# Performance work log

Hardware: AMD Instinct MI355X
Metric: run time of the kernel (lower is better)

The kernel has to match this reference:

```python
import jax, jax.numpy as jnp
import numpy as np


def setup_inputs() -> dict:
    key = jax.random.key(0)
    k1, k2 = jax.random.split(key)
    B, N, M, D = 4, 8192, 8192, 3
    ground_truth = jax.random.normal(k1, (B, N, D), dtype=jnp.float32)
    reconstruction = jax.random.normal(k2, (B, M, D), dtype=jnp.float32)
    return {"ground_truth": ground_truth, "reconstruction": reconstruction}


def reference(ground_truth, reconstruction):
    x, y = ground_truth, reconstruction  # [B,N,D], [B,M,D]
    xx = jnp.sum(x * x, axis=-1)                      # [B,N]
    yy = jnp.sum(y * y, axis=-1)                      # [B,M]
    xy = jnp.einsum('bnd,bmd->bnm', x, y)             # [B,N,M]
    P = xx[:, :, None] + yy[:, None, :] - 2.0 * xy    # [B,N,M]
    # clamp(min=1e-10) then mean, in both directions
    loss_1 = jnp.mean(jnp.maximum(jnp.min(P, axis=1), 1e-10))
    loss_2 = jnp.mean(jnp.maximum(jnp.min(P, axis=2), 1e-10))
    total = (loss_1 + loss_2) * 1000.0
    return total
```

## Files before the change

kernel.cpp:

```cpp
#include <hip/hip_runtime.h>

typedef _Float16 half_t;
typedef _Float16 f16x8 __attribute__((ext_vector_type(8)));
typedef float f32x16 __attribute__((ext_vector_type(16)));

#define BATCH 4
#define NPTS 8192
#define NSEG 128
#define MSEG 2048
#define CHUNK_M 512
#define NTILES 16
#define NCHUNKS (MSEG / CHUNK_M)

__global__ __launch_bounds__(256, 4) void chamfer_mfma_kernel(
    const float* __restrict__ gt, const float* __restrict__ rec,
    unsigned int* __restrict__ minbuf)
{
    const int nseg = blockIdx.x;
    const int mseg = blockIdx.y;
    const int b    = blockIdx.z;
    const float* G = gt  + (size_t)b * NPTS * 3;
    const float* R = rec + (size_t)b * NPTS * 3;
    const int n0 = nseg * NSEG;
    const int m0 = mseg * MSEG;

    const int tid  = threadIdx.x;
    const int lane = tid & 63;
    const int w    = tid >> 6;
    const int lr   = lane & 31;
    const int lh   = lane >> 5;

    __shared__ unsigned int rowbuf[MSEG];
    __shared__ float bfrag[NTILES][64][4];

    for (int i = tid; i < MSEG; i += 256) rowbuf[i] = 0x7F7F7F7Fu;
    for (int i = tid; i < NTILES * 32; i += 256) {
        int t = i >> 5, l = (i & 31) + 32;
        bfrag[t][l][0] = 0.f; bfrag[t][l][1] = 0.f;
        bfrag[t][l][2] = 0.f; bfrag[t][l][3] = 0.f;
    }

    f16x8 afrag = {};
    {
        int n = n0 + w * 32 + lr;
        float gx = G[n*3+0], gy = G[n*3+1], gz = G[n*3+2];
        half_t hx = (half_t)gx, hy = (half_t)gy, hz = (half_t)gz;
        float fx = (float)hx, fy = (float)hy, fz = (float)hz;
        float nrm = fx*fx + fy*fy + fz*fz;
        half_t nhi = (half_t)nrm;
        half_t nlo = (half_t)(nrm - (float)nhi);
        if (lh == 0) {
            afrag[0]=hx; afrag[1]=hy; afrag[2]=hz; afrag[3]=nhi;
            afrag[4]=nlo; afrag[5]=(half_t)1.f; afrag[6]=(half_t)1.f;
            afrag[7]=(half_t)0.f;
        }
    }

    f32x16 colacc;
    #pragma unroll
    for (int i = 0; i < 16; ++i) colacc[i] = 3.0e38f;

    const f32x16 zc = {};

    auto process = [&](const f32x16& d, int mbase) {
        #pragma unroll
        for (int i = 0; i < 16; ++i) colacc[i] = fminf(colacc[i], d[i]);
        float a0 = fminf(d[0], d[1]),   a1 = fminf(d[2], d[3]);
        float a2 = fminf(d[4], d[5]),   a3 = fminf(d[6], d[7]);
        float a4 = fminf(d[8], d[9]),   a5 = fminf(d[10], d[11]);
        float a6 = fminf(d[12], d[13]), a7 = fminf(d[14], d[15]);
        float b0 = fminf(a0, a1), b1 = fminf(a2, a3);
        float b2 = fminf(a4, a5), b3 = fminf(a6, a7);
        float rmin = fminf(fminf(b0, b1), fminf(b2, b3));
        atomicMin(&rowbuf[mbase + lr], __float_as_uint(rmin));
    };

    for (int ch = 0; ch < NCHUNKS; ++ch) {
        __syncthreads();
        #pragma unroll
        for (int s = 0; s < 2; ++s) {
            int j = tid * 2 + s;
            int m = m0 + ch * CHUNK_M + j;
            float rx = R[m*3+0], ry = R[m*3+1], rz = R[m*3+2];
            half_t hx = (half_t)rx, hy = (half_t)ry, hz = (half_t)rz;
            float fx = (float)hx, fy = (float)hy, fz = (float)hz;
            float nrm = fx*fx + fy*fy + fz*fz;
            half_t mhi = (half_t)nrm;
            half_t mlo = (half_t)(nrm - (float)mhi);
            union { half_t h[8]; float4 f4; } u;
            u.h[0] = (half_t)(-2.f*fx); u.h[1] = (half_t)(-2.f*fy);
            u.h[2] = (half_t)(-2.f*fz); u.h[3] = (half_t)1.f;
            u.h[4] = (half_t)1.f;       u.h[5] = mhi;
            u.h[6] = mlo;               u.h[7] = (half_t)0.f;
            int t = j >> 5, c = j & 31;
            *(float4*)&bfrag[t][c][0] = u.f4;
        }
        __syncthreads();

        f16x8 bf0 = *(const f16x8*)&bfrag[0][lane][0];
        f32x16 dprev = __builtin_amdgcn_mfma_f32_32x32x16_f16(afrag, bf0, zc, 0, 0, 0);
        #pragma unroll
        for (int t = 1; t < NTILES; ++t) {
            f16x8 bft = *(const f16x8*)&bfrag[t][lane][0];
            f32x16 dcur = __builtin_amdgcn_mfma_f32_32x32x16_f16(afrag, bft, zc, 0, 0, 0);
            process(dprev, ch * CHUNK_M + (t - 1) * 32);
            dprev = dcur;
        }
        process(dprev, ch * CHUNK_M + (NTILES - 1) * 32);
    }
    __syncthreads();

    unsigned int* mb0 = minbuf + (size_t)b * NPTS;
    for (int i = tid; i < MSEG; i += 256)
        atomicMin(&mb0[m0 + i], rowbuf[i]);

    #pragma unroll
    for (int i = 0; i < 16; ++i) {
        float v = colacc[i];
        v = fminf(v, __shfl_xor(v, 1));
        v = fminf(v, __shfl_xor(v, 2));
        v = fminf(v, __shfl_xor(v, 4));
        v = fminf(v, __shfl_xor(v, 8));
        v = fminf(v, __shfl_xor(v, 16));
        colacc[i] = v;
    }
    unsigned int* mb1 = minbuf + (size_t)(BATCH + b) * NPTS;
    if (lr == 0) {
        #pragma unroll
        for (int i = 0; i < 16; ++i) {
            int r = (i & 3) + 8 * (i >> 2) + 4 * lh;
            atomicMin(&mb1[n0 + w * 32 + r], __float_as_uint(colacc[i]));
        }
    }
}

__global__ __launch_bounds__(256) void chamfer_reduce_kernel(
    const unsigned int* __restrict__ minbuf, float* __restrict__ out)
{
    int idx = (blockIdx.x * 256 + threadIdx.x) * 4;
    uint4 v = *(const uint4*)&minbuf[idx];
    float s = fmaxf(__uint_as_float(v.x), 1e-10f)
            + fmaxf(__uint_as_float(v.y), 1e-10f)
            + fmaxf(__uint_as_float(v.z), 1e-10f)
            + fmaxf(__uint_as_float(v.w), 1e-10f);
    #pragma unroll
    for (int off = 32; off > 0; off >>= 1) s += __shfl_down(s, off);
    __shared__ float ws4[4];
    int wv = threadIdx.x >> 6, ln = threadIdx.x & 63;
    if (ln == 0) ws4[wv] = s;
    __syncthreads();
    if (threadIdx.x == 0) {
        float tot = ws4[0] + ws4[1] + ws4[2] + ws4[3];
        atomicAdd(out, tot * (1000.0f / 32768.0f));
    }
}

extern "C" void kernel_launch(void* const* d_in, const int* in_sizes, int n_in,
                              void* d_out, int out_size, void* d_ws, size_t ws_size,
                              hipStream_t stream) {
    const float* gt  = (const float*)d_in[0];
    const float* rec = (const float*)d_in[1];
    unsigned int* minbuf = (unsigned int*)d_ws;

    hipMemsetAsync(minbuf, 0x7F, (size_t)2 * BATCH * NPTS * sizeof(unsigned int), stream);
    hipMemsetAsync(d_out, 0, sizeof(float), stream);

    dim3 grid(NPTS / NSEG, NPTS / MSEG, BATCH);
    chamfer_mfma_kernel<<<grid, 256, 0, stream>>>(gt, rec, minbuf);
    chamfer_reduce_kernel<<<(2 * BATCH * NPTS) / (256 * 4), 256, 0, stream>>>(
        minbuf, (float*)d_out);
}
```

Measured before the change: 82.53 us.

## Use 32x32x8 f16 MFMA, larger chunks, prefetched loads, and a fused init kernel

Switches from the 32x32x16 MFMA, whose K dimension was half zero padding, to the 32x32x8 variant. The augmented 8-element vectors are split across the two half-waves, so the shared B fragments shrink to float2 per lane. It doubles the chunk size so the loop has fewer block syncs, and prefetches the next chunk's points into registers with vectorised float2 loads while the current chunk computes. It also processes tiles in pairs with fused min trees, and replaces the two memsets with a single init kernel. The cost is higher register pressure from the prefetch buffers and two live accumulators, which may limit occupancy at the requested launch bounds.

```diff
diff --git a/kernel.cpp b/kernel.cpp
--- a/kernel.cpp
+++ b/kernel.cpp
@@ -1,6 +1,7 @@
 #include <hip/hip_runtime.h>
 
 typedef _Float16 half_t;
+typedef _Float16 f16x4 __attribute__((ext_vector_type(4)));
 typedef _Float16 f16x8 __attribute__((ext_vector_type(8)));
 typedef float f32x16 __attribute__((ext_vector_type(16)));
 
@@ -8,9 +9,32 @@
 #define NPTS 8192
 #define NSEG 128
 #define MSEG 2048
-#define CHUNK_M 512
-#define NTILES 16
+#define CHUNK_M 1024
+#define NTILES 32
 #define NCHUNKS (MSEG / CHUNK_M)
+
+#if __has_builtin(__builtin_amdgcn_mfma_f32_32x32x8f16)
+static __device__ __forceinline__ f32x16 MFMA8(f16x4 a, f16x4 b, f32x16 c) {
+    return __builtin_amdgcn_mfma_f32_32x32x8f16(a, b, c, 0, 0, 0);
+}
+#else
+static __device__ __forceinline__ f32x16 MFMA8(f16x4 a, f16x4 b, f32x16 c) {
+    f16x8 a8 = {a[0], a[1], a[2], a[3], (half_t)0.f, (half_t)0.f, (half_t)0.f, (half_t)0.f};
+    f16x8 b8 = {b[0], b[1], b[2], b[3], (half_t)0.f, (half_t)0.f, (half_t)0.f, (half_t)0.f};
+    return __builtin_amdgcn_mfma_f32_32x32x16_f16(a8, b8, c, 0, 0, 0);
+}
+#endif
+
+static __device__ __forceinline__ float tree16(const f32x16& d) {
+    float t0 = fminf(fminf(d[0], d[1]), d[2]);
+    float t1 = fminf(fminf(d[3], d[4]), d[5]);
+    float t2 = fminf(fminf(d[6], d[7]), d[8]);
+    float t3 = fminf(fminf(d[9], d[10]), d[11]);
+    float t4 = fminf(fminf(d[12], d[13]), d[14]);
+    float u0 = fminf(fminf(t0, t1), t2);
+    float u1 = fminf(fminf(t3, t4), d[15]);
+    return fminf(u0, u1);
+}
 
 __global__ __launch_bounds__(256, 4) void chamfer_mfma_kernel(
     const float* __restrict__ gt, const float* __restrict__ rec,
@@ -31,16 +55,11 @@
     const int lh   = lane >> 5;
 
     __shared__ unsigned int rowbuf[MSEG];
-    __shared__ float bfrag[NTILES][64][4];
+    __shared__ float2 bfrag[NTILES][64];
 
     for (int i = tid; i < MSEG; i += 256) rowbuf[i] = 0x7F7F7F7Fu;
-    for (int i = tid; i < NTILES * 32; i += 256) {
-        int t = i >> 5, l = (i & 31) + 32;
-        bfrag[t][l][0] = 0.f; bfrag[t][l][1] = 0.f;
-        bfrag[t][l][2] = 0.f; bfrag[t][l][3] = 0.f;
-    }
-
-    f16x8 afrag = {};
+
+    f16x4 afrag;
     {
         int n = n0 + w * 32 + lr;
         float gx = G[n*3+0], gy = G[n*3+1], gz = G[n*3+2];
@@ -49,64 +68,78 @@
         float nrm = fx*fx + fy*fy + fz*fz;
         half_t nhi = (half_t)nrm;
         half_t nlo = (half_t)(nrm - (float)nhi);
-        if (lh == 0) {
-            afrag[0]=hx; afrag[1]=hy; afrag[2]=hz; afrag[3]=nhi;
-            afrag[4]=nlo; afrag[5]=(half_t)1.f; afrag[6]=(half_t)1.f;
-            afrag[7]=(half_t)0.f;
-        }
+        if (lh == 0) { afrag[0]=hx;  afrag[1]=hy;          afrag[2]=hz;          afrag[3]=nhi; }
+        else         { afrag[0]=nlo; afrag[1]=(half_t)1.f; afrag[2]=(half_t)1.f; afrag[3]=(half_t)0.f; }
     }
 
     f32x16 colacc;
     #pragma unroll
     for (int i = 0; i < 16; ++i) colacc[i] = 3.0e38f;
-
     const f32x16 zc = {};
 
-    auto process = [&](const f32x16& d, int mbase) {
-        #pragma unroll
-        for (int i = 0; i < 16; ++i) colacc[i] = fminf(colacc[i], d[i]);
-        float a0 = fminf(d[0], d[1]),   a1 = fminf(d[2], d[3]);
-        float a2 = fminf(d[4], d[5]),   a3 = fminf(d[6], d[7]);
-        float a4 = fminf(d[8], d[9]),   a5 = fminf(d[10], d[11]);
-        float a6 = fminf(d[12], d[13]), a7 = fminf(d[14], d[15]);
-        float b0 = fminf(a0, a1), b1 = fminf(a2, a3);
-        float b2 = fminf(a4, a5), b3 = fminf(a6, a7);
-        float rmin = fminf(fminf(b0, b1), fminf(b2, b3));
-        atomicMin(&rowbuf[mbase + lr], __float_as_uint(rmin));
+    float2 pref[6];
+    auto loadpts = [&](int ch) {
+        int m = m0 + ch * CHUNK_M + tid * 4;
+        const float2* p = (const float2*)R + (size_t)(m * 3) / 2;
+        #pragma unroll
+        for (int k = 0; k < 6; ++k) pref[k] = p[k];
     };
-
-    for (int ch = 0; ch < NCHUNKS; ++ch) {
-        __syncthreads();
-        #pragma unroll
-        for (int s = 0; s < 2; ++s) {
-            int j = tid * 2 + s;
-            int m = m0 + ch * CHUNK_M + j;
-            float rx = R[m*3+0], ry = R[m*3+1], rz = R[m*3+2];
-            half_t hx = (half_t)rx, hy = (half_t)ry, hz = (half_t)rz;
+    auto writepack = [&]() {
+        float px[4], py[4], pz[4];
+        px[0]=pref[0].x; py[0]=pref[0].y; pz[0]=pref[1].x;
+        px[1]=pref[1].y; py[1]=pref[2].x; pz[1]=pref[2].y;
+        px[2]=pref[3].x; py[2]=pref[3].y; pz[2]=pref[4].x;
+        px[3]=pref[4].y; py[3]=pref[5].x; pz[3]=pref[5].y;
+        #pragma unroll
+        for (int s = 0; s < 4; ++s) {
+            int j = tid * 4 + s;
+            half_t hx = (half_t)px[s], hy = (half_t)py[s], hz = (half_t)pz[s];
             float fx = (float)hx, fy = (float)hy, fz = (float)hz;
             float nrm = fx*fx + fy*fy + fz*fz;
             half_t mhi = (half_t)nrm;
             half_t mlo = (half_t)(nrm - (float)mhi);
-            union { half_t h[8]; float4 f4; } u;
-            u.h[0] = (half_t)(-2.f*fx); u.h[1] = (half_t)(-2.f*fy);
-            u.h[2] = (half_t)(-2.f*fz); u.h[3] = (half_t)1.f;
-            u.h[4] = (half_t)1.f;       u.h[5] = mhi;
-            u.h[6] = mlo;               u.h[7] = (half_t)0.f;
+            union { half_t h[4]; float2 f; } u0, u1;
+            u0.h[0] = (half_t)(-2.f*fx); u0.h[1] = (half_t)(-2.f*fy);
+            u0.h[2] = (half_t)(-2.f*fz); u0.h[3] = (half_t)1.f;
+            u1.h[0] = (half_t)1.f; u1.h[1] = mhi; u1.h[2] = mlo; u1.h[3] = (half_t)0.f;
             int t = j >> 5, c = j & 31;
-            *(float4*)&bfrag[t][c][0] = u.f4;
+            bfrag[t][c]      = u0.f;
+            bfrag[t][c + 32] = u1.f;
         }
+    };
+
+    auto process2 = [&](const f32x16& da, const f32x16& db, int mba, int mbb) {
+        #pragma unroll
+        for (int i = 0; i < 16; ++i)
+            colacc[i] = fminf(fminf(colacc[i], da[i]), db[i]);
+        atomicMin(&rowbuf[mba + lr], __float_as_uint(tree16(da)));
+        atomicMin(&rowbuf[mbb + lr], __float_as_uint(tree16(db)));
+    };
+
+    union { float2 f; f16x4 h; } cv;
+
+    loadpts(0);
+    for (int ch = 0; ch < NCHUNKS; ++ch) {
         __syncthreads();
-
-        f16x8 bf0 = *(const f16x8*)&bfrag[0][lane][0];
-        f32x16 dprev = __builtin_amdgcn_mfma_f32_32x32x16_f16(afrag, bf0, zc, 0, 0, 0);
-        #pragma unroll
-        for (int t = 1; t < NTILES; ++t) {
-            f16x8 bft = *(const f16x8*)&bfrag[t][lane][0];
-            f32x16 dcur = __builtin_amdgcn_mfma_f32_32x32x16_f16(afrag, bft, zc, 0, 0, 0);
-            process(dprev, ch * CHUNK_M + (t - 1) * 32);
-            dprev = dcur;
+        writepack();
+        __syncthreads();
+        if (ch + 1 < NCHUNKS) loadpts(ch + 1);
+        const int mbase = ch * CHUNK_M;
+
+        cv.f = bfrag[0][lane]; f16x4 b0 = cv.h;
+        cv.f = bfrag[1][lane]; f16x4 b1 = cv.h;
+        f32x16 d0 = MFMA8(afrag, b0, zc);
+        f32x16 d1 = MFMA8(afrag, b1, zc);
+        #pragma unroll
+        for (int t = 2; t < NTILES; t += 2) {
+            cv.f = bfrag[t][lane];     f16x4 ba = cv.h;
+            cv.f = bfrag[t + 1][lane]; f16x4 bb = cv.h;
+            f32x16 na = MFMA8(afrag, ba, zc);
+            f32x16 nb = MFMA8(afrag, bb, zc);
+            process2(d0, d1, mbase + (t - 2) * 32, mbase + (t - 1) * 32);
+            d0 = na; d1 = nb;
         }
-        process(dprev, ch * CHUNK_M + (NTILES - 1) * 32);
+        process2(d0, d1, mbase + (NTILES - 2) * 32, mbase + (NTILES - 1) * 32);
     }
     __syncthreads();
 
@@ -132,6 +165,14 @@
             atomicMin(&mb1[n0 + w * 32 + r], __float_as_uint(colacc[i]));
         }
     }
+}
+
+__global__ __launch_bounds__(256) void chamfer_init_kernel(
+    unsigned int* __restrict__ minbuf, float* __restrict__ out)
+{
+    int idx = (blockIdx.x * 256 + threadIdx.x) * 4;
+    *(uint4*)&minbuf[idx] = make_uint4(0x7F7F7F7Fu, 0x7F7F7F7Fu, 0x7F7F7F7Fu, 0x7F7F7F7Fu);
+    if (blockIdx.x == 0 && threadIdx.x == 0) out[0] = 0.0f;
 }
 
 __global__ __launch_bounds__(256) void chamfer_reduce_kernel(
@@ -162,11 +203,11 @@
     const float* rec = (const float*)d_in[1];
     unsigned int* minbuf = (unsigned int*)d_ws;
 
-    hipMemsetAsync(minbuf, 0x7F, (size_t)2 * BATCH * NPTS * sizeof(unsigned int), stream);
-    hipMemsetAsync(d_out, 0, sizeof(float), stream);
+    const int TOT = 2 * BATCH * NPTS;
+    chamfer_init_kernel<<<TOT / (256 * 4), 256, 0, stream>>>(minbuf, (float*)d_out);
 
     dim3 grid(NPTS / NSEG, NPTS / MSEG, BATCH);
     chamfer_mfma_kernel<<<grid, 256, 0, stream>>>(gt, rec, minbuf);
-    chamfer_reduce_kernel<<<(2 * BATCH * NPTS) / (256 * 4), 256, 0, stream>>>(
-        minbuf, (float*)d_out);
-}
+
+    chamfer_reduce_kernel<<<TOT / (256 * 4), 256, 0, stream>>>(minbuf, (float*)d_out);
+}
```

After: 74.81 us. 1.1x faster.
